# Optimization experiments

Measured on AMD Instinct MI355X. Metric: run time of the kernel, lower is better.

The kernel has to match this reference:

```python
import jax, jax.numpy as jnp
import numpy as np

D = 1024
H = 16
HD = D // H
EPS = 1e-6


def rms_norm(x, w):
    # x: [..., hd]; compute in float32 like the torch module
    xf = x.astype(jnp.float32)
    rms = jnp.sqrt(jnp.mean(xf * xf, axis=-1, keepdims=True) + EPS)
    return (xf / rms * w.astype(jnp.float32)).astype(x.dtype)


def setup_inputs() -> dict:
    key = jax.random.key(0)
    ks = jax.random.split(key, 6)
    B, S = 2, 2048
    x = jax.random.normal(ks[0], (B, S, D), dtype=jnp.float32)
    Wqkv = jax.random.normal(ks[1], (3 * D, D), dtype=jnp.float32) * (1.0 / np.sqrt(D))
    bqkv = jax.random.normal(ks[2], (3 * D,), dtype=jnp.float32) * 0.02
    Wproj = jax.random.normal(ks[3], (D, D), dtype=jnp.float32) * (1.0 / np.sqrt(D))
    bproj = jax.random.normal(ks[4], (D,), dtype=jnp.float32) * 0.02
    qn_w = jnp.ones((HD,), dtype=jnp.float32)
    kn_w = jnp.ones((HD,), dtype=jnp.float32)
    return {"x": x, "Wqkv": Wqkv, "bqkv": bqkv, "Wproj": Wproj, "bproj": bproj,
            "qn_w": qn_w, "kn_w": kn_w}


def reference(x, Wqkv, bqkv, Wproj, bproj, qn_w, kn_w):
    B, S, _ = x.shape
    # QKV projection: torch Linear is x @ W.T + b
    qkv = x @ Wqkv.T + bqkv                     # [B, S, 3D]
    qkv = qkv.reshape(B, S, 3, H, HD)
    q, k, v = qkv[:, :, 0], qkv[:, :, 1], qkv[:, :, 2]   # each [B, S, H, hd]
    q = rms_norm(q, qn_w)
    k = rms_norm(k, kn_w)
    # move heads forward: [B, H, S, hd]
    q = q.transpose(0, 2, 1, 3)
    k = k.transpose(0, 2, 1, 3)
    v = v.transpose(0, 2, 1, 3)
    scale = 1.0 / np.sqrt(HD)
    scores = jnp.einsum('bhsd,bhtd->bhst', q, k) * scale   # [B, H, S, S] (math backend)
    attn = jax.nn.softmax(scores, axis=-1)
    out = jnp.einsum('bhst,bhtd->bhsd', attn, v)            # [B, H, S, hd]
    out = out.transpose(0, 2, 1, 3).reshape(B, S, D)
    return out @ Wproj.T + bproj
```

## Files before the change

kernel.cpp:

```cpp
#include <hip/hip_runtime.h>
#include <hip/hip_bf16.h>
#include <math.h>

#define D_MODEL 1024
#define NH 16
#define HD 64
#define SEQ 2048
#define BATCH 2
#define NTOK (BATCH*SEQ)

typedef short bf16x8 __attribute__((ext_vector_type(8)));
typedef short s4 __attribute__((ext_vector_type(4)));
typedef float f32x4 __attribute__((ext_vector_type(4)));
typedef unsigned short us4 __attribute__((ext_vector_type(4)));

#define MFMA(a,b,c) __builtin_amdgcn_mfma_f32_16x16x32_bf16(a,b,c,0,0,0)

union bfu { __hip_bfloat16 b; unsigned short u; };
__device__ __forceinline__ unsigned short f2b(float f){ bfu t; t.b = __float2bfloat16(f); return t.u; }
__device__ __forceinline__ float b2f(unsigned short u){ bfu t; t.u = u; return __bfloat162float(t.b); }
__device__ __forceinline__ unsigned short f2bf(float f){
    unsigned int u = __float_as_uint(f);
    u += 0x7FFFu + ((u >> 16) & 1u);
    return (unsigned short)(u >> 16);
}

__device__ __forceinline__ void g2l16(const unsigned short* g, unsigned short* l){
    __builtin_amdgcn_global_load_lds(
        (const __attribute__((address_space(1))) unsigned int*)g,
        (__attribute__((address_space(3))) unsigned int*)l, 16, 0, 0);
}

#define OFF_X   128L
#define OFF_WQ  (OFF_X  + 4194304L)
#define OFF_BQ  (OFF_WQ + 3145728L)
#define OFF_WP  (OFF_BQ + 3072L)
#define OFF_BP  (OFF_WP + 1048576L)
#define OFF_QN  (OFF_BP + 1024L)
#define OFF_KN  (OFF_QN + 64L)
#define OFF_Q   (OFF_KN + 64L)
#define OFF_K   (OFF_Q  + 4194304L)
#define OFF_V   (OFF_K  + 4194304L)
#define OFF_A   (OFF_V  + 4194304L)


__global__ __launch_bounds__(256) void detect_kernel(
    const unsigned int* __restrict__ xraw, int* __restrict__ cnt)
{
    int i = blockIdx.x*256 + threadIdx.x;
    uint4 v = ((const uint4*)xraw)[i];
    unsigned int w[4] = {v.x, v.y, v.z, v.w};
    int local = 0;
    #pragma unroll
    for (int j=0;j<4;j++){
        local += ((w[j] & 0x7F80u) >= 0x4800u);
        local += (((w[j]>>16) & 0x7F80u) >= 0x4800u);
    }
    if (local) atomicAdd(cnt, local);
}

__global__ __launch_bounds__(256) void convert_kernel(
    const void* __restrict__ x,  const void* __restrict__ wq,
    const void* __restrict__ bq, const void* __restrict__ wp,
    const void* __restrict__ bp, const void* __restrict__ qn,
    const void* __restrict__ kn, unsigned short* __restrict__ ws,
    const int* __restrict__ cntp)
{
    const int flag = (*cntp > 256);
    long i = (long)blockIdx.x*blockDim.x + threadIdx.x;
    const long stride = (long)gridDim.x*blockDim.x;
    const long NCH = 2098208L;
    for (; i < NCH; i += stride){
        long j = i; const void* src; long off;
        if (j < 1048576L)                  { src = x;  off = OFF_X;  }
        else if ((j -= 1048576L) < 786432L){ src = wq; off = OFF_WQ; }
        else if ((j -= 786432L)  < 768L)   { src = bq; off = OFF_BQ; }
        else if ((j -= 768L)     < 262144L){ src = wp; off = OFF_WP; }
        else if ((j -= 262144L)  < 256L)   { src = bp; off = OFF_BP; }
        else if ((j -= 256L)     < 16L)    { src = qn; off = OFF_QN; }
        else      { j -= 16L;                src = kn; off = OFF_KN; }
        us4 o;
        if (flag){
            float4 v = ((const float4*)src)[j];
            o.x = f2b(v.x); o.y = f2b(v.y); o.z = f2b(v.z); o.w = f2b(v.w);
        } else {
            o = ((const us4*)src)[j];
        }
        *(us4*)(ws + off + j*4) = o;
    }
}

__global__ __launch_bounds__(256) void qkv_kernel(
    const unsigned short* __restrict__ x,
    const unsigned short* __restrict__ Wqkv,
    const unsigned short* __restrict__ bqkv,
    const unsigned short* __restrict__ qn_w,
    const unsigned short* __restrict__ kn_w,
    unsigned short* __restrict__ qbuf,
    unsigned short* __restrict__ kbuf,
    unsigned short* __restrict__ vbuf)
{
    __shared__ __align__(16) unsigned short tA[128*32];
    __shared__ __align__(16) unsigned short tB[128*32];
    const int tid  = threadIdx.x;
    const int w    = tid >> 6, lane = tid & 63, quad = lane >> 4, c = lane & 15;
    const int m0 = blockIdx.y*128, n0 = blockIdx.x*128;
    const int am = (w>>1)*64, bn = (w&1)*64;

    f32x4 acc[4][4];
    for (int mi=0;mi<4;mi++) for (int ni=0;ni<4;ni++) acc[mi][ni] = {0.f,0.f,0.f,0.f};

    const int i0 = tid, i1 = tid + 256;
    const long ga0 = (long)(m0 + (i0>>2))*D_MODEL + (i0&3)*8;
    const long ga1 = (long)(m0 + (i1>>2))*D_MODEL + (i1&3)*8;
    const long gb0 = (long)(n0 + (i0>>2))*D_MODEL + (i0&3)*8;
    const long gb1 = (long)(n0 + (i1>>2))*D_MODEL + (i1&3)*8;

    for (int k0=0;k0<D_MODEL;k0+=32){
        g2l16(x    + ga0 + k0, tA + i0*8);
        g2l16(x    + ga1 + k0, tA + i1*8);
        g2l16(Wqkv + gb0 + k0, tB + i0*8);
        g2l16(Wqkv + gb1 + k0, tB + i1*8);
        __syncthreads();
        bf16x8 a[4], b[4];
        for (int mi=0;mi<4;mi++) a[mi] = *(const bf16x8*)(tA + (am + mi*16 + c)*32 + quad*8);
        for (int ni=0;ni<4;ni++) b[ni] = *(const bf16x8*)(tB + (bn + ni*16 + c)*32 + quad*8);
        for (int mi=0;mi<4;mi++)
            for (int ni=0;ni<4;ni++)
                acc[mi][ni] = MFMA(a[mi], b[ni], acc[mi][ni]);
        __syncthreads();
    }

    const int nw = n0 + bn, mw = m0 + am;
    const int region = nw >> 10;
    const int h      = (nw & 1023) >> 6;
    float bias[4], wn[4];
    for (int ni=0;ni<4;ni++){
        bias[ni] = b2f(bqkv[nw + ni*16 + c]);
        wn[ni]   = 1.0f;
    }
    if (region==0) for (int ni=0;ni<4;ni++) wn[ni] = b2f(qn_w[ni*16+c]);
    if (region==1) for (int ni=0;ni<4;ni++) wn[ni] = b2f(kn_w[ni*16+c]);

    for (int mi=0;mi<4;mi++){
        for (int ni=0;ni<4;ni++)
            for (int r=0;r<4;r++) acc[mi][ni][r] += bias[ni];

        float scale_r[4];
        if (region < 2){
            for (int r=0;r<4;r++){
                float ss = 0.f;
                for (int ni=0;ni<4;ni++){ float v2 = acc[mi][ni][r]; ss += v2*v2; }
                ss += __shfl_xor(ss, 1, 64);
                ss += __shfl_xor(ss, 2, 64);
                ss += __shfl_xor(ss, 4, 64);
                ss += __shfl_xor(ss, 8, 64);
                scale_r[r] = rsqrtf(ss*(1.0f/64.0f) + 1e-6f);
            }
        } else {
            for (int r=0;r<4;r++) scale_r[r] = 1.0f;
        }

        for (int r=0;r<4;r++){
            int m = mw + mi*16 + quad*4 + r;
            int bidx = m >> 11, s = m & 2047;
            long bb = (long)(bidx*NH + h)*SEQ*HD;
            if (region == 0){
                long base = bb + (long)s*HD;
                for (int ni=0;ni<4;ni++)
                    qbuf[base + ni*16 + c] = f2bf(acc[mi][ni][r] * scale_r[r] * wn[ni]);
            } else if (region == 1){
                long tb = bb + (long)(s>>6)*4096;
                for (int ni=0;ni<4;ni++){
                    int d = ni*16 + c;
                    long idx = tb + (long)((s&63)*8 + ((d>>3) ^ (s&7)))*8 + (d&7);
                    kbuf[idx] = f2bf(acc[mi][ni][r] * scale_r[r] * wn[ni]);
                }
            } else {
                long tb = bb + (long)(s>>6)*4096;
                for (int ni=0;ni<4;ni++){
                    int d = ni*16 + c;
                    long idx = tb + (long)(d*8 + (((s>>3)&7) ^ (d&7)))*8 + (s&7);
                    vbuf[idx] = f2bf(acc[mi][ni][r]);
                }
            }
        }
    }
}

__global__ __launch_bounds__(256, 4) void attn_kernel(
    const unsigned short* __restrict__ qbuf,
    const unsigned short* __restrict__ kts,
    const unsigned short* __restrict__ vts,
    unsigned short* __restrict__ abuf)
{
    const int tid = threadIdx.x, w = tid>>6, lane = tid&63, quad = lane>>4, c = lane&15;
    const int bh = blockIdx.y, qt = blockIdx.x;
    const unsigned short* qb = qbuf + (long)bh*SEQ*HD;
    const unsigned short* kb = kts + (long)bh*SEQ*HD;
    const unsigned short* vb = vts + (long)bh*SEQ*HD;
    const int qbase = qt*64 + w*16;
    const int cq = c & 7;

    __shared__ __align__(16) unsigned short KT[2][4096];
    __shared__ __align__(16) unsigned short VT[2][4096];
    __shared__ __align__(16) unsigned short P[4][1024];
    unsigned short* Pw = &P[w][0];

    bf16x8 aq[2];
    #pragma unroll
    for (int ks=0;ks<2;ks++)
        aq[ks] = *(const bf16x8*)(qb + (long)(qbase + c)*HD + ks*32 + quad*8);

    bf16x8 onesf;
    #pragma unroll
    for (int j=0;j<8;j++) onesf[j] = (short)0x3F80;

    f32x4 o[4], o4;
    #pragma unroll
    for (int nt=0;nt<4;nt++) o[nt] = {0.f,0.f,0.f,0.f};
    o4 = {0.f,0.f,0.f,0.f};

    auto stage = [&](const unsigned short* src, unsigned short* dst){
        g2l16(src + tid*8,        dst + tid*8);
        g2l16(src + 2048 + tid*8, dst + 2048 + tid*8);
    };

    stage(kb, KT[0]); stage(vb, VT[0]);
    __syncthreads();

    for (int kt2=0; kt2<SEQ/64; kt2++){
        const unsigned short* ktl = KT[kt2&1];
        const unsigned short* vtl = VT[kt2&1];
        if (kt2 < SEQ/64 - 1){
            stage(kb + (kt2+1)*4096, KT[(kt2&1)^1]);
            stage(vb + (kt2+1)*4096, VT[(kt2&1)^1]);
        }

        bf16x8 kf[4][2];
        #pragma unroll
        for (int mt=0;mt<4;mt++)
            #pragma unroll
            for (int ks=0;ks<2;ks++)
                kf[mt][ks] = *(const bf16x8*)(ktl + ((mt*16+c)*8 + ((ks*4+quad)^cq))*8);

        f32x4 z4[4];
        #pragma unroll
        for (int mt=0;mt<4;mt++){
            f32x4 t = {0.f,0.f,0.f,0.f};
            t = MFMA(kf[mt][0], aq[0], t);
            t = MFMA(kf[mt][1], aq[1], t);
            z4[mt] = t;
        }

        #pragma unroll
        for (int mt=0;mt<4;mt++){
            const int key8 = mt*2 + (quad>>1);
            unsigned int u0 = __float_as_uint(exp2f(z4[mt][0]*0.18033688f - 17.312340f));
            unsigned int u1 = __float_as_uint(exp2f(z4[mt][1]*0.18033688f - 17.312340f));
            unsigned int u2 = __float_as_uint(exp2f(z4[mt][2]*0.18033688f - 17.312340f));
            unsigned int u3 = __float_as_uint(exp2f(z4[mt][3]*0.18033688f - 17.312340f));
            uint2 pk;
            pk.x = __builtin_amdgcn_perm(u1, u0, 0x07060302u);
            pk.y = __builtin_amdgcn_perm(u3, u2, 0x07060302u);
            *(uint2*)(Pw + key8*128 + c*8 + (quad&1)*4) = pk;
        }

        #pragma unroll
        for (int ks=0;ks<2;ks++){
            bf16x8 bv[4];
            #pragma unroll
            for (int nt=0;nt<4;nt++)
                bv[nt] = *(const bf16x8*)(vtl + ((nt*16+c)*8 + ((ks*4+quad)^cq))*8);
            bf16x8 ap = *(const bf16x8*)(Pw + (ks*4+quad)*128 + c*8);
            #pragma unroll
            for (int nt=0;nt<4;nt++)
                o[nt] = MFMA(ap, bv[nt], o[nt]);
            o4 = MFMA(ap, onesf, o4);
        }
        __syncthreads();
    }

    const int b = bh >> 4, h = bh & 15;
    #pragma unroll
    for (int r=0;r<4;r++){
        float inv = 1.0f / o4[r];
        int s = qbase + quad*4 + r;
        long base = ((long)(b*SEQ + s)*NH + h)*HD;
        #pragma unroll
        for (int nt=0;nt<4;nt++)
            abuf[base + nt*16 + c] = f2bf(o[nt][r]*inv);
    }
}

__global__ __launch_bounds__(256) void proj_kernel(
    const unsigned short* __restrict__ abuf,
    const unsigned short* __restrict__ Wp,
    const unsigned short* __restrict__ bp,
    void* __restrict__ outv,
    const int* __restrict__ cntp)
{
    __shared__ __align__(16) unsigned short tA[128*32];
    __shared__ __align__(16) unsigned short tB[64*32];
    const int tid  = threadIdx.x;
    const int w    = tid >> 6, lane = tid & 63, quad = lane >> 4, c = lane & 15;
    const int m0 = blockIdx.y*128, n0 = blockIdx.x*64;
    const int am = (w>>1)*64, bn = (w&1)*32;
    const int flag = (*cntp > 256);

    f32x4 acc[4][2];
    for (int mi=0;mi<4;mi++) for (int ni=0;ni<2;ni++) acc[mi][ni] = {0.f,0.f,0.f,0.f};

    const int i0 = tid, i1 = tid + 256;
    const long ga0 = (long)(m0 + (i0>>2))*D_MODEL + (i0&3)*8;
    const long ga1 = (long)(m0 + (i1>>2))*D_MODEL + (i1&3)*8;
    const long gb0 = (long)(n0 + (i0>>2))*D_MODEL + (i0&3)*8;

    for (int k0=0;k0<D_MODEL;k0+=32){
        g2l16(abuf + ga0 + k0, tA + i0*8);
        g2l16(abuf + ga1 + k0, tA + i1*8);
        g2l16(Wp   + gb0 + k0, tB + i0*8);
        __syncthreads();
        bf16x8 a[4], b[2];
        for (int mi=0;mi<4;mi++) a[mi] = *(const bf16x8*)(tA + (am + mi*16 + c)*32 + quad*8);
        for (int ni=0;ni<2;ni++) b[ni] = *(const bf16x8*)(tB + (bn + ni*16 + c)*32 + quad*8);
        for (int mi=0;mi<4;mi++)
            for (int ni=0;ni<2;ni++)
                acc[mi][ni] = MFMA(a[mi], b[ni], acc[mi][ni]);
        __syncthreads();
    }

    float bias[2];
    for (int ni=0;ni<2;ni++) bias[ni] = b2f(bp[n0 + bn + ni*16 + c]);

    for (int mi=0;mi<4;mi++)
        for (int r=0;r<4;r++){
            long m = m0 + am + mi*16 + quad*4 + r;
            for (int ni=0;ni<2;ni++){
                float val = acc[mi][ni][r] + bias[ni];
                long idx = m*D_MODEL + n0 + bn + ni*16 + c;
                if (flag) ((float*)outv)[idx] = val;
                else      ((unsigned short*)outv)[idx] = f2bf(val);
            }
        }
}

extern "C" void kernel_launch(void* const* d_in, const int* in_sizes, int n_in,
                              void* d_out, int out_size, void* d_ws, size_t ws_size,
                              hipStream_t stream)
{
    unsigned short* ws = (unsigned short*)d_ws;
    int* cnt = (int*)d_ws;

    hipMemsetAsync(cnt, 0, 4, stream);
    hipLaunchKernelGGL(detect_kernel, dim3(16), dim3(256), 0, stream,
                       (const unsigned int*)d_in[0], cnt);
    hipLaunchKernelGGL(convert_kernel, dim3(2048), dim3(256), 0, stream,
                       d_in[0], d_in[1], d_in[2], d_in[3], d_in[4], d_in[5], d_in[6],
                       ws, cnt);
    hipLaunchKernelGGL(qkv_kernel,  dim3(24,32), dim3(256), 0, stream,
                       ws+OFF_X, ws+OFF_WQ, ws+OFF_BQ, ws+OFF_QN, ws+OFF_KN,
                       ws+OFF_Q, ws+OFF_K, ws+OFF_V);
    hipLaunchKernelGGL(attn_kernel, dim3(32,32), dim3(256), 0, stream,
                       ws+OFF_Q, ws+OFF_K, ws+OFF_V, ws+OFF_A);
    hipLaunchKernelGGL(proj_kernel, dim3(16,32), dim3(256), 0, stream,
                       ws+OFF_A, ws+OFF_WP, ws+OFF_BP, d_out, cnt);
}
```

Baseline: 219.5 us.

## Fuse dtype detection into kernels, fold softmax scale into Q, vectorize QKV stores

Removes the separate memset and detect kernel by having each block of convert and proj independently scan a small slice of x in shared memory to decide fp32 vs bf16. The QKV epilogue computes transposed MFMA tiles (B×A) so each lane owns four contiguous head dims, allowing packed 8-byte stores for Q, K and V and a cheaper RMS reduction. The softmax scale log2e/sqrt(hd) is folded into Q at normalization so attention skips a multiply per score. The max-offset constant is also dropped from exp2, which relies on the scores of the normalized q and k staying bounded, and the detection heuristic now uses a much smaller sample.

Measured after the change: 222.1 us. No clear change (+1.2%).

```diff
diff --git a/kernel.cpp b/kernel.cpp
--- a/kernel.cpp
+++ b/kernel.cpp
@@ -44,29 +44,25 @@
 #define OFF_A   (OFF_V  + 4194304L)
 
 
-__global__ __launch_bounds__(256) void detect_kernel(
-    const unsigned int* __restrict__ xraw, int* __restrict__ cnt)
-{
-    int i = blockIdx.x*256 + threadIdx.x;
-    uint4 v = ((const uint4*)xraw)[i];
-    unsigned int w[4] = {v.x, v.y, v.z, v.w};
-    int local = 0;
-    #pragma unroll
-    for (int j=0;j<4;j++){
-        local += ((w[j] & 0x7F80u) >= 0x4800u);
-        local += (((w[j]>>16) & 0x7F80u) >= 0x4800u);
-    }
-    if (local) atomicAdd(cnt, local);
+__device__ __forceinline__ int detect_flag(const unsigned short* xraw, int tid){
+    __shared__ int cnt;
+    if (tid == 0) cnt = 0;
+    __syncthreads();
+    uint2 v = ((const uint2*)xraw)[tid];
+    int loc = ((v.x & 0x7F80u) >= 0x4800u) + (((v.x>>16) & 0x7F80u) >= 0x4800u)
+            + ((v.y & 0x7F80u) >= 0x4800u) + (((v.y>>16) & 0x7F80u) >= 0x4800u);
+    if (loc) atomicAdd(&cnt, loc);
+    __syncthreads();
+    return cnt > 4;
 }
 
 __global__ __launch_bounds__(256) void convert_kernel(
     const void* __restrict__ x,  const void* __restrict__ wq,
     const void* __restrict__ bq, const void* __restrict__ wp,
     const void* __restrict__ bp, const void* __restrict__ qn,
-    const void* __restrict__ kn, unsigned short* __restrict__ ws,
-    const int* __restrict__ cntp)
-{
-    const int flag = (*cntp > 256);
+    const void* __restrict__ kn, unsigned short* __restrict__ ws)
+{
+    const int flag = detect_flag((const unsigned short*)x, threadIdx.x);
     long i = (long)blockIdx.x*blockDim.x + threadIdx.x;
     const long stride = (long)gridDim.x*blockDim.x;
     const long NCH = 2098208L;
@@ -106,9 +102,10 @@
     const int w    = tid >> 6, lane = tid & 63, quad = lane >> 4, c = lane & 15;
     const int m0 = blockIdx.y*128, n0 = blockIdx.x*128;
     const int am = (w>>1)*64, bn = (w&1)*64;
+    const int region = n0 >> 10;
 
     f32x4 acc[4][4];
-    for (int mi=0;mi<4;mi++) for (int ni=0;ni<4;ni++) acc[mi][ni] = {0.f,0.f,0.f,0.f};
+    for (int i=0;i<4;i++) for (int j=0;j<4;j++) acc[i][j] = {0.f,0.f,0.f,0.f};
 
     const int i0 = tid, i1 = tid + 256;
     const long ga0 = (long)(m0 + (i0>>2))*D_MODEL + (i0&3)*8;
@@ -116,73 +113,94 @@
     const long gb0 = (long)(n0 + (i0>>2))*D_MODEL + (i0&3)*8;
     const long gb1 = (long)(n0 + (i1>>2))*D_MODEL + (i1&3)*8;
 
-    for (int k0=0;k0<D_MODEL;k0+=32){
-        g2l16(x    + ga0 + k0, tA + i0*8);
-        g2l16(x    + ga1 + k0, tA + i1*8);
-        g2l16(Wqkv + gb0 + k0, tB + i0*8);
-        g2l16(Wqkv + gb1 + k0, tB + i1*8);
-        __syncthreads();
-        bf16x8 a[4], b[4];
-        for (int mi=0;mi<4;mi++) a[mi] = *(const bf16x8*)(tA + (am + mi*16 + c)*32 + quad*8);
-        for (int ni=0;ni<4;ni++) b[ni] = *(const bf16x8*)(tB + (bn + ni*16 + c)*32 + quad*8);
-        for (int mi=0;mi<4;mi++)
+    if (region < 2){
+        for (int k0=0;k0<D_MODEL;k0+=32){
+            g2l16(x    + ga0 + k0, tA + i0*8);
+            g2l16(x    + ga1 + k0, tA + i1*8);
+            g2l16(Wqkv + gb0 + k0, tB + i0*8);
+            g2l16(Wqkv + gb1 + k0, tB + i1*8);
+            __syncthreads();
+            bf16x8 a[4], b[4];
+            for (int mi=0;mi<4;mi++) a[mi] = *(const bf16x8*)(tA + (am + mi*16 + c)*32 + quad*8);
+            for (int ni=0;ni<4;ni++) b[ni] = *(const bf16x8*)(tB + (bn + ni*16 + c)*32 + quad*8);
             for (int ni=0;ni<4;ni++)
-                acc[mi][ni] = MFMA(a[mi], b[ni], acc[mi][ni]);
-        __syncthreads();
-    }
-
-    const int nw = n0 + bn, mw = m0 + am;
-    const int region = nw >> 10;
-    const int h      = (nw & 1023) >> 6;
-    float bias[4], wn[4];
-    for (int ni=0;ni<4;ni++){
-        bias[ni] = b2f(bqkv[nw + ni*16 + c]);
-        wn[ni]   = 1.0f;
-    }
-    if (region==0) for (int ni=0;ni<4;ni++) wn[ni] = b2f(qn_w[ni*16+c]);
-    if (region==1) for (int ni=0;ni<4;ni++) wn[ni] = b2f(kn_w[ni*16+c]);
-
-    for (int mi=0;mi<4;mi++){
-        for (int ni=0;ni<4;ni++)
-            for (int r=0;r<4;r++) acc[mi][ni][r] += bias[ni];
-
-        float scale_r[4];
-        if (region < 2){
-            for (int r=0;r<4;r++){
-                float ss = 0.f;
-                for (int ni=0;ni<4;ni++){ float v2 = acc[mi][ni][r]; ss += v2*v2; }
-                ss += __shfl_xor(ss, 1, 64);
-                ss += __shfl_xor(ss, 2, 64);
-                ss += __shfl_xor(ss, 4, 64);
-                ss += __shfl_xor(ss, 8, 64);
-                scale_r[r] = rsqrtf(ss*(1.0f/64.0f) + 1e-6f);
-            }
-        } else {
-            for (int r=0;r<4;r++) scale_r[r] = 1.0f;
-        }
-
-        for (int r=0;r<4;r++){
-            int m = mw + mi*16 + quad*4 + r;
-            int bidx = m >> 11, s = m & 2047;
-            long bb = (long)(bidx*NH + h)*SEQ*HD;
+                for (int mi=0;mi<4;mi++)
+                    acc[ni][mi] = MFMA(b[ni], a[mi], acc[ni][mi]);
+            __syncthreads();
+        }
+
+        const int h = ((n0 + bn) & 1023) >> 6;
+        const unsigned short* nwp = (region==0) ? qn_w : kn_w;
+        const float qs = (region==0) ? 0.18033688f : 1.0f;
+        float wnv[4][4], bias[4][4];
+        for (int ni=0;ni<4;ni++){
+            us4 wv = *(const us4*)(nwp + ni*16 + quad*4);
+            us4 bv = *(const us4*)(bqkv + n0 + bn + ni*16 + quad*4);
+            for (int r=0;r<4;r++){ wnv[ni][r] = b2f(wv[r]); bias[ni][r] = b2f(bv[r]); }
+        }
+
+        for (int mi=0;mi<4;mi++){
+            float ss = 0.f;
+            for (int ni=0;ni<4;ni++)
+                for (int r=0;r<4;r++){
+                    acc[ni][mi][r] += bias[ni][r];
+                    ss += acc[ni][mi][r]*acc[ni][mi][r];
+                }
+            ss += __shfl_xor(ss, 16, 64);
+            ss += __shfl_xor(ss, 32, 64);
+            const float sc = rsqrtf(ss*(1.0f/64.0f) + 1e-6f) * qs;
+
+            const int token = m0 + am + mi*16 + c;
+            const int bidx = token >> 11, s = token & 2047;
             if (region == 0){
-                long base = bb + (long)s*HD;
-                for (int ni=0;ni<4;ni++)
-                    qbuf[base + ni*16 + c] = f2bf(acc[mi][ni][r] * scale_r[r] * wn[ni]);
-            } else if (region == 1){
-                long tb = bb + (long)(s>>6)*4096;
+                long base = ((long)(bidx*NH + h)*SEQ + s)*HD + quad*4;
                 for (int ni=0;ni<4;ni++){
-                    int d = ni*16 + c;
-                    long idx = tb + (long)((s&63)*8 + ((d>>3) ^ (s&7)))*8 + (d&7);
-                    kbuf[idx] = f2bf(acc[mi][ni][r] * scale_r[r] * wn[ni]);
+                    us4 pk;
+                    for (int r=0;r<4;r++) pk[r] = f2bf(acc[ni][mi][r]*sc*wnv[ni][r]);
+                    *(us4*)(qbuf + base + ni*16) = pk;
                 }
             } else {
-                long tb = bb + (long)(s>>6)*4096;
+                long tb = (long)(bidx*NH + h)*SEQ*HD + (long)(s>>6)*4096;
+                const int kl = s & 63;
                 for (int ni=0;ni<4;ni++){
-                    int d = ni*16 + c;
-                    long idx = tb + (long)(d*8 + (((s>>3)&7) ^ (d&7)))*8 + (s&7);
-                    vbuf[idx] = f2bf(acc[mi][ni][r]);
+                    int slot = kl*8 + ((ni*2 + (quad>>1)) ^ (kl & 7));
+                    us4 pk;
+                    for (int r=0;r<4;r++) pk[r] = f2bf(acc[ni][mi][r]*sc*wnv[ni][r]);
+                    *(us4*)(kbuf + tb + slot*8 + (quad&1)*4) = pk;
                 }
+            }
+        }
+    } else {
+        for (int k0=0;k0<D_MODEL;k0+=32){
+            g2l16(x    + ga0 + k0, tA + i0*8);
+            g2l16(x    + ga1 + k0, tA + i1*8);
+            g2l16(Wqkv + gb0 + k0, tB + i0*8);
+            g2l16(Wqkv + gb1 + k0, tB + i1*8);
+            __syncthreads();
+            bf16x8 a[4], b[4];
+            for (int mi=0;mi<4;mi++) a[mi] = *(const bf16x8*)(tA + (am + mi*16 + c)*32 + quad*8);
+            for (int ni=0;ni<4;ni++) b[ni] = *(const bf16x8*)(tB + (bn + ni*16 + c)*32 + quad*8);
+            for (int mi=0;mi<4;mi++)
+                for (int ni=0;ni<4;ni++)
+                    acc[mi][ni] = MFMA(a[mi], b[ni], acc[mi][ni]);
+            __syncthreads();
+        }
+
+        const int h = ((n0 + bn) & 1023) >> 6;
+        float bias[4];
+        for (int ni=0;ni<4;ni++) bias[ni] = b2f(bqkv[n0 + bn + ni*16 + c]);
+
+        const int bidx = (m0 + am) >> 11;
+        const int sbase = (m0 + am) & 2047;
+        for (int mi=0;mi<4;mi++){
+            long tb = (long)(bidx*NH + h)*SEQ*HD + (long)(sbase>>6)*4096;
+            const int klhi = (mi*2 + (quad>>1)) & 7;
+            for (int ni=0;ni<4;ni++){
+                const int d = ni*16 + c;
+                int chunk = d*8 + (klhi ^ (d & 7));
+                us4 pk;
+                for (int r=0;r<4;r++) pk[r] = f2bf(acc[mi][ni][r] + bias[ni]);
+                *(us4*)(vbuf + tb + chunk*8 + (quad&1)*4) = pk;
             }
         }
     }
@@ -256,10 +274,10 @@
         #pragma unroll
         for (int mt=0;mt<4;mt++){
             const int key8 = mt*2 + (quad>>1);
-            unsigned int u0 = __float_as_uint(exp2f(z4[mt][0]*0.18033688f - 17.312340f));
-            unsigned int u1 = __float_as_uint(exp2f(z4[mt][1]*0.18033688f - 17.312340f));
-            unsigned int u2 = __float_as_uint(exp2f(z4[mt][2]*0.18033688f - 17.312340f));
-            unsigned int u3 = __float_as_uint(exp2f(z4[mt][3]*0.18033688f - 17.312340f));
+            unsigned int u0 = __float_as_uint(exp2f(z4[mt][0]));
+            unsigned int u1 = __float_as_uint(exp2f(z4[mt][1]));
+            unsigned int u2 = __float_as_uint(exp2f(z4[mt][2]));
+            unsigned int u3 = __float_as_uint(exp2f(z4[mt][3]));
             uint2 pk;
             pk.x = __builtin_amdgcn_perm(u1, u0, 0x07060302u);
             pk.y = __builtin_amdgcn_perm(u3, u2, 0x07060302u);
@@ -298,15 +316,15 @@
     const unsigned short* __restrict__ Wp,
     const unsigned short* __restrict__ bp,
     void* __restrict__ outv,
-    const int* __restrict__ cntp)
+    const unsigned short* __restrict__ xraw)
 {
     __shared__ __align__(16) unsigned short tA[128*32];
     __shared__ __align__(16) unsigned short tB[64*32];
     const int tid  = threadIdx.x;
+    const int flag = detect_flag(xraw, tid);
     const int w    = tid >> 6, lane = tid & 63, quad = lane >> 4, c = lane & 15;
     const int m0 = blockIdx.y*128, n0 = blockIdx.x*64;
     const int am = (w>>1)*64, bn = (w&1)*32;
-    const int flag = (*cntp > 256);
 
     f32x4 acc[4][2];
     for (int mi=0;mi<4;mi++) for (int ni=0;ni<2;ni++) acc[mi][ni] = {0.f,0.f,0.f,0.f};
@@ -350,19 +368,16 @@
                               hipStream_t stream)
 {
     unsigned short* ws = (unsigned short*)d_ws;
-    int* cnt = (int*)d_ws;
-
-    hipMemsetAsync(cnt, 0, 4, stream);
-    hipLaunchKernelGGL(detect_kernel, dim3(16), dim3(256), 0, stream,
-                       (const unsigned int*)d_in[0], cnt);
+
     hipLaunchKernelGGL(convert_kernel, dim3(2048), dim3(256), 0, stream,
                        d_in[0], d_in[1], d_in[2], d_in[3], d_in[4], d_in[5], d_in[6],
-                       ws, cnt);
+                       ws);
     hipLaunchKernelGGL(qkv_kernel,  dim3(24,32), dim3(256), 0, stream,
                        ws+OFF_X, ws+OFF_WQ, ws+OFF_BQ, ws+OFF_QN, ws+OFF_KN,
                        ws+OFF_Q, ws+OFF_K, ws+OFF_V);
     hipLaunchKernelGGL(attn_kernel, dim3(32,32), dim3(256), 0, stream,
                        ws+OFF_Q, ws+OFF_K, ws+OFF_V, ws+OFF_A);
     hipLaunchKernelGGL(proj_kernel, dim3(16,32), dim3(256), 0, stream,
-                       ws+OFF_A, ws+OFF_WP, ws+OFF_BP, d_out, cnt);
-}
+                       ws+OFF_A, ws+OFF_WP, ws+OFF_BP, d_out,
+                       (const unsigned short*)d_in[0]);
+}
```
